# Kernel optimization log

Measured on AMD Instinct MI355X. Metric: run time of the kernel, lower is better.

The kernel has to match this reference:

```python
import jax, jax.numpy as jnp
import numpy as np

NUM_EMBEDDINGS = 1024
EMBEDDING_DIM = 64
DECAY = 0.99
EPS = 1e-5


def setup_inputs() -> dict:
    key = jax.random.key(0)
    k0, k1, k2 = jax.random.split(key, 3)
    return {
        "inputs": jax.random.normal(k0, (32, 64, 64, EMBEDDING_DIM), dtype=jnp.float32),
        "embeddings": jax.random.normal(k1, (NUM_EMBEDDINGS, EMBEDDING_DIM), dtype=jnp.float32),
        "ema_cluster_size": jnp.ones((NUM_EMBEDDINGS,), dtype=jnp.float32),
        "ema_w": jax.random.normal(k2, (NUM_EMBEDDINGS, EMBEDDING_DIM), dtype=jnp.float32),
    }


def reference(inputs, embeddings, ema_cluster_size, ema_w):
    input_shape = inputs.shape
    flat = inputs.reshape(-1, EMBEDDING_DIM)  # [N, D]

    input_sq = jnp.sum(flat * flat, axis=1, keepdims=True)          # [N, 1]
    codebook_sq = jnp.sum(embeddings * embeddings, axis=1)          # [K]
    dot = jnp.matmul(flat, embeddings.T)                            # [N, K]
    distances = input_sq + codebook_sq - 2.0 * dot

    encoding_indices = jnp.argmin(distances, axis=-1)               # [N]
    encodings = jax.nn.one_hot(encoding_indices, NUM_EMBEDDINGS, dtype=flat.dtype)  # [N, K]
    quantized_flat = jnp.take(embeddings, encoding_indices, axis=0)  # [N, D]

    # --- EMA updates (training path) ---
    current_counts = jax.ops.segment_sum(
        jnp.ones_like(encoding_indices, dtype=flat.dtype),
        encoding_indices, num_segments=NUM_EMBEDDINGS)              # == sum(encodings, 0)
    upd_cluster = ema_cluster_size * DECAY + (1.0 - DECAY) * current_counts
    n = jnp.sum(upd_cluster)
    upd_cluster = (upd_cluster + EPS) / (n + NUM_EMBEDDINGS * EPS) * n

    # sum of inputs assigned to each code == encodings.T @ flat
    assignment_sums = jax.ops.segment_sum(flat, encoding_indices,
                                          num_segments=NUM_EMBEDDINGS)  # [K, D]
    upd_ema_w = ema_w * DECAY + (1.0 - DECAY) * assignment_sums
    upd_embeddings = upd_ema_w / (upd_cluster[:, None] + EPS)

    quantization_loss = jnp.mean((flat - quantized_flat) ** 2).reshape((1,))
    quantized = quantized_flat.reshape(input_shape)
    quantized_flow = inputs + jax.lax.stop_gradient(quantized - inputs)

    usage_counts = current_counts
    usage_ratio = jnp.sum((usage_counts > 0).astype(jnp.float32)) / NUM_EMBEDDINGS

    return (quantized_flow, encodings, usage_ratio, quantization_loss,
            upd_embeddings, upd_cluster, upd_ema_w)
```

## Files before the change

### kernel.cpp

```cpp
#include <hip/hip_runtime.h>
#include <hip/hip_bf16.h>

#define NK 1024
#define ND 64
#define NV 131072
#define BR 128
#define DECAY_F 0.99f
#define OMD_F 0.01f
#define EPS_F 1e-5f
#define KEPS_F 0.01024f

typedef const __attribute__((address_space(1))) void* gas1_t;
typedef __attribute__((address_space(3))) void* las3_t;
#define GLOAD_LDS16(gp, lp) \
    __builtin_amdgcn_global_load_lds((gas1_t)(gp), (las3_t)(lp), 16, 0, 0)


__global__ __launch_bounds__(256) void vq_prep(const float* __restrict__ emb,
                                               float* __restrict__ csq,
                                               int* __restrict__ cnt,
                                               double* loss,
                                               float4* __restrict__ acc4)
{
    int k = blockIdx.x * 256 + threadIdx.x;
    cnt[k] = 0;
    if (k == 0) *loss = 0.0;
    float4 z = make_float4(0.f, 0.f, 0.f, 0.f);
#pragma unroll
    for (int i = 0; i < 16; ++i) acc4[k + i * 1024] = z;
    float p[ND];
    const float4* e4 = reinterpret_cast<const float4*>(emb + (size_t)k * ND);
#pragma unroll
    for (int i = 0; i < 16; ++i) {
        float4 v = e4[i];
        p[4*i+0] = __fmul_rn(v.x, v.x);
        p[4*i+1] = __fmul_rn(v.y, v.y);
        p[4*i+2] = __fmul_rn(v.z, v.z);
        p[4*i+3] = __fmul_rn(v.w, v.w);
    }
    float r[8];
#pragma unroll
    for (int j = 0; j < 8; ++j) r[j] = p[j];
#pragma unroll
    for (int i = 8; i < ND; i += 8)
#pragma unroll
        for (int j = 0; j < 8; ++j) r[j] = __fadd_rn(r[j], p[i+j]);
    csq[k] = __fadd_rn(__fadd_rn(__fadd_rn(r[0], r[1]), __fadd_rn(r[2], r[3])),
                       __fadd_rn(__fadd_rn(r[4], r[5]), __fadd_rn(r[6], r[7])));
}

__global__ __launch_bounds__(256, 2) void vq_assign(
    const float* __restrict__ x_in, const float* __restrict__ emb,
    const float* __restrict__ csq, float* __restrict__ out_qf,
    float* __restrict__ out_enc, int* __restrict__ indices,
    int* __restrict__ cnt, double* __restrict__ loss_acc)
{
    __shared__ __align__(16) float xs[BR * ND];
    __shared__ __align__(16) float es[128 * ND];
    __shared__ float csq_s[NK];
    __shared__ float isq_s[BR];
    __shared__ double lds_ls[4];

    const int tid  = threadIdx.x;
    const int lane = tid & 63;
    const int wv   = tid >> 6;
    const int tx   = tid & 15;
    const int ty   = tid >> 4;
    const int txs  = tx & 7;
    const int tys  = ty & 7;
    const size_t rowbase = (size_t)blockIdx.x * BR;

#pragma unroll
    for (int c = 0; c < 8; ++c) {
        int f = tid + c * 256;
        int row = f >> 4, ch = f & 15;
        int sch = ch ^ (row & 7);
        GLOAD_LDS16(x_in + rowbase * ND + row * ND + sch * 4, &xs[f * 4]);
    }
#pragma unroll
    for (int c = 0; c < 8; ++c) {
        int f = tid + c * 256;
        int row = f >> 4, ch = f & 15;
        int sch = ch ^ (row & 7);
        GLOAD_LDS16(emb + (size_t)row * ND + sch * 4, &es[f * 4]);
    }
#pragma unroll
    for (int c = 0; c < 4; ++c) csq_s[tid + c * 256] = csq[tid + c * 256];
    __syncthreads();

    if (tid < BR) {
        const int rs = tid & 7;
        const float* xr = &xs[tid * ND];
        float r[8];
        {
            float4 a = *(const float4*)&xr[(0 ^ rs) * 4];
            float4 b = *(const float4*)&xr[(1 ^ rs) * 4];
            r[0] = __fmul_rn(a.x, a.x); r[1] = __fmul_rn(a.y, a.y);
            r[2] = __fmul_rn(a.z, a.z); r[3] = __fmul_rn(a.w, a.w);
            r[4] = __fmul_rn(b.x, b.x); r[5] = __fmul_rn(b.y, b.y);
            r[6] = __fmul_rn(b.z, b.z); r[7] = __fmul_rn(b.w, b.w);
        }
#pragma unroll
        for (int g = 1; g < 8; ++g) {
            float4 a = *(const float4*)&xr[((2*g)   ^ rs) * 4];
            float4 b = *(const float4*)&xr[((2*g+1) ^ rs) * 4];
            r[0] = __fadd_rn(r[0], __fmul_rn(a.x, a.x));
            r[1] = __fadd_rn(r[1], __fmul_rn(a.y, a.y));
            r[2] = __fadd_rn(r[2], __fmul_rn(a.z, a.z));
            r[3] = __fadd_rn(r[3], __fmul_rn(a.w, a.w));
            r[4] = __fadd_rn(r[4], __fmul_rn(b.x, b.x));
            r[5] = __fadd_rn(r[5], __fmul_rn(b.y, b.y));
            r[6] = __fadd_rn(r[6], __fmul_rn(b.z, b.z));
            r[7] = __fadd_rn(r[7], __fmul_rn(b.w, b.w));
        }
        isq_s[tid] = __fadd_rn(__fadd_rn(__fadd_rn(r[0], r[1]), __fadd_rn(r[2], r[3])),
                               __fadd_rn(__fadd_rn(r[4], r[5]), __fadd_rn(r[6], r[7])));
    }

    float best[8];
    int   bestk[8];
#pragma unroll
    for (int i = 0; i < 8; ++i) { best[i] = 3.4e38f; bestk[i] = 0; }

    for (int t = 0; t < 8; ++t) {
        float acc[8][8];
#pragma unroll
        for (int i = 0; i < 8; ++i)
#pragma unroll
            for (int j = 0; j < 8; ++j) acc[i][j] = 0.f;

        for (int ch = 0; ch < 16; ++ch) {
            const int xo = (ch ^ tys) * 4;
            const int eo = (ch ^ txs) * 4;
            float4 xf[8], ef[8];
#pragma unroll
            for (int i = 0; i < 8; ++i)
                xf[i] = *(const float4*)&xs[(ty + 16*i) * ND + xo];
#pragma unroll
            for (int j = 0; j < 8; ++j)
                ef[j] = *(const float4*)&es[(tx + 16*j) * ND + eo];
#pragma unroll
            for (int i = 0; i < 8; ++i) {
#pragma unroll
                for (int j = 0; j < 8; ++j) {
                    float a = acc[i][j];
                    a = __builtin_fmaf(xf[i].x, ef[j].x, a);
                    a = __builtin_fmaf(xf[i].y, ef[j].y, a);
                    a = __builtin_fmaf(xf[i].z, ef[j].z, a);
                    a = __builtin_fmaf(xf[i].w, ef[j].w, a);
                    acc[i][j] = a;
                }
            }
        }

#pragma unroll
        for (int i = 0; i < 8; ++i) {
            float isq = isq_s[ty + 16*i];
#pragma unroll
            for (int j = 0; j < 8; ++j) {
                float dist = __fsub_rn(__fadd_rn(isq, csq_s[t * 128 + tx + 16*j]),
                                       __fmul_rn(2.0f, acc[i][j]));
                if (dist < best[i]) { best[i] = dist; bestk[i] = t * 128 + tx + 16*j; }
            }
        }

        {
            int rl = t * 16 + wv * 4;
#pragma unroll
            for (int rr = 0; rr < 4; ++rr) {
                float4* dst = reinterpret_cast<float4*>(out_enc + (rowbase + rl + rr) * NK);
                float4 z = make_float4(0.f, 0.f, 0.f, 0.f);
#pragma unroll
                for (int jj = 0; jj < 4; ++jj) dst[jj * 64 + lane] = z;
            }
        }

        __syncthreads();
        if (t < 7) {
#pragma unroll
            for (int c = 0; c < 8; ++c) {
                int f = tid + c * 256;
                int row = f >> 4, ch = f & 15;
                int sch = ch ^ (row & 7);
                GLOAD_LDS16(emb + (size_t)(t + 1) * 128 * ND + row * ND + sch * 4,
                            &es[f * 4]);
            }
        }
        __syncthreads();
    }

    float* red_d = es;
    int*   red_i = reinterpret_cast<int*>(es + 2048);
#pragma unroll
    for (int i = 0; i < 8; ++i) {
        red_d[(ty + 16*i) * 16 + tx] = best[i];
        red_i[(ty + 16*i) * 16 + tx] = bestk[i];
    }
    __syncthreads();
    if (tid < BR) {
        float bd = red_d[tid * 16];
        int   bk = red_i[tid * 16];
#pragma unroll
        for (int c = 1; c < 16; ++c) {
            float d  = red_d[tid * 16 + c];
            int   k2 = red_i[tid * 16 + c];
            if (d < bd || (d == bd && k2 < bk)) { bd = d; bk = k2; }
        }
        size_t grow = rowbase + tid;
        indices[grow] = bk;
        out_enc[grow * NK + bk] = 1.0f;
        atomicAdd(&cnt[bk], 1);
        red_i[tid * 16] = bk;
    }
    __syncthreads();

    float lsum = 0.f;
    const int lsw = ((lane >> 2)) ;
    for (int r = 0; r < 32; ++r) {
        int rl = wv * 32 + r;
        int kr = red_i[rl * 16];
        size_t grow = rowbase + rl;
        float xv = xs[rl * ND + ((lsw ^ (rl & 7)) << 2) + (lane & 3)];
        float ev = emb[(size_t)kr * ND + lane];
        out_qf[grow * ND + lane] = __fadd_rn(xv, __fsub_rn(ev, xv));
        float dd = __fsub_rn(xv, ev);
        lsum = __builtin_fmaf(dd, dd, lsum);
    }
    double ls = (double)lsum;
#pragma unroll
    for (int off = 32; off >= 1; off >>= 1) ls += __shfl_xor(ls, off, 64);
    if (lane == 0) lds_ls[wv] = ls;
    __syncthreads();
    if (tid == 0)
        atomicAdd(loss_acc, (lds_ls[0] + lds_ls[1]) + (lds_ls[2] + lds_ls[3]));
}

__global__ __launch_bounds__(256) void vq_scan(
    const int* __restrict__ cnt, const float* __restrict__ ema_cs,
    const double* __restrict__ loss_acc, float* __restrict__ ucf_ws,
    int* __restrict__ base, int* __restrict__ cursor,
    float* __restrict__ out_uc, float* __restrict__ out_usage,
    float* __restrict__ out_loss)
{
    __shared__ float uc_s[1024];
    __shared__ int   wsum[4];
    __shared__ int   usage_s;
    __shared__ float n_s;
    const int tid  = threadIdx.x;
    const int lane = tid & 63;
    const int wv   = tid >> 6;
    if (tid == 0) usage_s = 0;
    __syncthreads();

    int c4[4];
    int ucount = 0;
#pragma unroll
    for (int j = 0; j < 4; ++j) {
        int k = tid * 4 + j;
        int c = cnt[k];
        c4[j] = c;
        if (c > 0) ucount++;
        uc_s[k] = __fadd_rn(__fmul_rn(ema_cs[k], DECAY_F), __fmul_rn(OMD_F, (float)c));
    }
    atomicAdd(&usage_s, ucount);
    __syncthreads();

    if (tid < 64) {
        int b = tid >> 3, j = tid & 7;
        float r = uc_s[b * 128 + j];
#pragma unroll
        for (int i = 1; i < 16; ++i)
            r = __fadd_rn(r, uc_s[b * 128 + 8 * i + j]);
        r = __fadd_rn(r, __shfl_xor(r, 1, 64));
        r = __fadd_rn(r, __shfl_xor(r, 2, 64));
        r = __fadd_rn(r, __shfl_xor(r, 4, 64));
        r = __fadd_rn(r, __shfl_xor(r, 8, 64));
        r = __fadd_rn(r, __shfl_xor(r, 16, 64));
        r = __fadd_rn(r, __shfl_xor(r, 32, 64));
        if (tid == 0) {
            n_s = r;
            *out_usage = __fdiv_rn((float)usage_s, 1024.0f);
            *out_loss  = (float)(*loss_acc / 8388608.0);
        }
    }
    __syncthreads();

    const float n = n_s;
#pragma unroll
    for (int j = 0; j < 4; ++j) {
        int k = tid * 4 + j;
        float ucfv = __fmul_rn(__fdiv_rn(__fadd_rn(uc_s[k], EPS_F), __fadd_rn(n, KEPS_F)), n);
        out_uc[k] = ucfv;
        ucf_ws[k] = ucfv;
    }

    int s = c4[0] + c4[1] + c4[2] + c4[3];
    int incl = s;
#pragma unroll
    for (int off = 1; off < 64; off <<= 1) {
        int v = __shfl_up(incl, off, 64);
        if (lane >= off) incl += v;
    }
    if (lane == 63) wsum[wv] = incl;
    __syncthreads();
    int woff = 0;
    for (int w = 0; w < wv; ++w) woff += wsum[w];
    int run = woff + incl - s;
#pragma unroll
    for (int j = 0; j < 4; ++j) {
        int k = tid * 4 + j;
        base[k] = run; cursor[k] = run;
        run += c4[j];
    }
}

__global__ __launch_bounds__(256) void vq_scatter(
    const int* __restrict__ idx, int* __restrict__ cursor,
    int* __restrict__ rows, int* __restrict__ codes)
{
    int i = blockIdx.x * 256 + threadIdx.x;
    int k = idx[i];
    int slot = atomicAdd(&cursor[k], 1);
    rows[slot] = i;
    codes[slot] = k;
}

__global__ __launch_bounds__(256) void vq_gather(
    const float* __restrict__ x_in, const int* __restrict__ rows,
    const int* __restrict__ codes, float* __restrict__ acc_buf)
{
    const int lane = threadIdx.x & 63;
    const int wv   = threadIdx.x >> 6;
    const int seg  = blockIdx.x * 4 + wv;
    const int g    = seg * 64;

    const int rid = rows[g + lane];
    const int kc  = codes[g + lane];

    float acc = 0.f;
    for (int e8 = 0; e8 < 8; ++e8) {
        float xv[8];
#pragma unroll
        for (int u = 0; u < 8; ++u) {
            int r = __shfl(rid, e8 * 8 + u, 64);
            xv[u] = x_in[(size_t)r * ND + lane];
        }
#pragma unroll
        for (int u = 0; u < 8; ++u) {
            int e = e8 * 8 + u;
            int k = __shfl(kc, e, 64);
            acc = __fadd_rn(acc, xv[u]);
            int knext = __shfl(kc, (e + 1) & 63, 64);
            if (e == 63) knext = -1;
            if (k != knext) {
                atomicAdd(&acc_buf[(size_t)k * ND + lane], acc);
                acc = 0.f;
            }
        }
    }
}

__global__ __launch_bounds__(256) void vq_final(
    const float* __restrict__ acc_buf, const float* __restrict__ ema_w,
    const float* __restrict__ ucf, float* __restrict__ out_updw,
    float* __restrict__ out_upde)
{
    int gid = blockIdx.x * 256 + threadIdx.x;
    int k = gid >> 6;
    float w = __fadd_rn(__fmul_rn(ema_w[gid], DECAY_F), __fmul_rn(OMD_F, acc_buf[gid]));
    out_updw[gid] = w;
    out_upde[gid] = __fdiv_rn(w, __fadd_rn(ucf[k], EPS_F));
}

extern "C" void kernel_launch(void* const* d_in, const int* in_sizes, int n_in,
                              void* d_out, int out_size, void* d_ws, size_t ws_size,
                              hipStream_t stream)
{
    const float* x_in   = (const float*)d_in[0];
    const float* emb    = (const float*)d_in[1];
    const float* ema_cs = (const float*)d_in[2];
    const float* ema_w  = (const float*)d_in[3];

    float* out_qf    = (float*)d_out;
    float* out_enc   = out_qf + (size_t)NV * ND;
    float* out_usage = out_enc + (size_t)NV * NK;
    float* out_loss  = out_usage + 1;
    float* out_upde  = out_loss + 1;
    float* out_uc    = out_upde + (size_t)NK * ND;
    float* out_updw  = out_uc + NK;

    char* ws = (char*)d_ws;
    float*  ws_csq    = (float*)(ws);
    int*    ws_cnt    = (int*)(ws + 4096);
    int*    ws_base   = (int*)(ws + 8192);
    int*    ws_cursor = (int*)(ws + 12288);
    float*  ws_ucf    = (float*)(ws + 16384);
    double* ws_loss   = (double*)(ws + 20480);
    int*    ws_idx    = (int*)(ws + 24576);
    int*    ws_rows   = (int*)(ws + 24576 + (size_t)NV * 4);
    int*    ws_codes  = (int*)(ws + 24576 + (size_t)NV * 8);
    float*  ws_acc    = (float*)(ws + 24576 + (size_t)NV * 12);

    vq_prep<<<4, 256, 0, stream>>>(emb, ws_csq, ws_cnt, ws_loss, (float4*)ws_acc);
    vq_assign<<<NV / BR, 256, 0, stream>>>(x_in, emb, ws_csq, out_qf, out_enc,
                                           ws_idx, ws_cnt, ws_loss);
    vq_scan<<<1, 256, 0, stream>>>(ws_cnt, ema_cs, ws_loss, ws_ucf, ws_base,
                                   ws_cursor, out_uc, out_usage, out_loss);
    vq_scatter<<<NV / 256, 256, 0, stream>>>(ws_idx, ws_cursor, ws_rows, ws_codes);
    vq_gather<<<512, 256, 0, stream>>>(x_in, ws_rows, ws_codes, ws_acc);
    vq_final<<<256, 256, 0, stream>>>(ws_acc, ema_w, ws_ucf, out_updw, out_upde);
}
```

Before: 322.2 us.

## Fuse per-code input sums into assign kernel via atomics, drop scatter/gather

Removes the scan-offset, scatter and gather kernels and accumulates assigned inputs into the per-code sum buffer with float atomics directly in the assign epilogue. It also moves the one-hot zero fill from inside the codebook tile loop into the epilogue, writing each row's zeros before setting the 1.0 after a memory wait and barrier. This cuts two launches and the re-read of inputs. In exchange it adds contended global float atomics and changes the order of floating-point summation.

Measured after the change: 300.0 us. 1.07x faster.

```diff
diff --git a/kernel.cpp b/kernel.cpp
--- a/kernel.cpp
+++ b/kernel.cpp
@@ -52,7 +52,7 @@
 __global__ __launch_bounds__(256, 2) void vq_assign(
     const float* __restrict__ x_in, const float* __restrict__ emb,
     const float* __restrict__ csq, float* __restrict__ out_qf,
-    float* __restrict__ out_enc, int* __restrict__ indices,
+    float* __restrict__ out_enc, float* __restrict__ acc_buf,
     int* __restrict__ cnt, double* __restrict__ loss_acc)
 {
     __shared__ __align__(16) float xs[BR * ND];
@@ -164,17 +164,6 @@
             }
         }
 
-        {
-            int rl = t * 16 + wv * 4;
-#pragma unroll
-            for (int rr = 0; rr < 4; ++rr) {
-                float4* dst = reinterpret_cast<float4*>(out_enc + (rowbase + rl + rr) * NK);
-                float4 z = make_float4(0.f, 0.f, 0.f, 0.f);
-#pragma unroll
-                for (int jj = 0; jj < 4; ++jj) dst[jj * 64 + lane] = z;
-            }
-        }
-
         __syncthreads();
         if (t < 7) {
 #pragma unroll
@@ -206,31 +195,40 @@
             int   k2 = red_i[tid * 16 + c];
             if (d < bd || (d == bd && k2 < bk)) { bd = d; bk = k2; }
         }
-        size_t grow = rowbase + tid;
-        indices[grow] = bk;
-        out_enc[grow * NK + bk] = 1.0f;
         atomicAdd(&cnt[bk], 1);
         red_i[tid * 16] = bk;
     }
     __syncthreads();
 
     float lsum = 0.f;
-    const int lsw = ((lane >> 2)) ;
+    const int lsw = (lane >> 2);
+    const float4 zv = make_float4(0.f, 0.f, 0.f, 0.f);
     for (int r = 0; r < 32; ++r) {
         int rl = wv * 32 + r;
         int kr = red_i[rl * 16];
         size_t grow = rowbase + rl;
+        float4* dst = reinterpret_cast<float4*>(out_enc + grow * NK);
+#pragma unroll
+        for (int jj = 0; jj < 4; ++jj) dst[jj * 64 + lane] = zv;
         float xv = xs[rl * ND + ((lsw ^ (rl & 7)) << 2) + (lane & 3)];
         float ev = emb[(size_t)kr * ND + lane];
         out_qf[grow * ND + lane] = __fadd_rn(xv, __fsub_rn(ev, xv));
         float dd = __fsub_rn(xv, ev);
         lsum = __builtin_fmaf(dd, dd, lsum);
+        atomicAdd(&acc_buf[(size_t)kr * ND + lane], xv);
     }
     double ls = (double)lsum;
 #pragma unroll
     for (int off = 32; off >= 1; off >>= 1) ls += __shfl_xor(ls, off, 64);
     if (lane == 0) lds_ls[wv] = ls;
-    __syncthreads();
+
+    asm volatile("s_waitcnt vmcnt(0)" ::: "memory");
+    __syncthreads();
+
+    if (tid < BR) {
+        int bk = red_i[tid * 16];
+        out_enc[(rowbase + tid) * NK + bk] = 1.0f;
+    }
     if (tid == 0)
         atomicAdd(loss_acc, (lds_ls[0] + lds_ls[1]) + (lds_ls[2] + lds_ls[3]));
 }
@@ -238,27 +236,21 @@
 __global__ __launch_bounds__(256) void vq_scan(
     const int* __restrict__ cnt, const float* __restrict__ ema_cs,
     const double* __restrict__ loss_acc, float* __restrict__ ucf_ws,
-    int* __restrict__ base, int* __restrict__ cursor,
     float* __restrict__ out_uc, float* __restrict__ out_usage,
     float* __restrict__ out_loss)
 {
     __shared__ float uc_s[1024];
-    __shared__ int   wsum[4];
     __shared__ int   usage_s;
     __shared__ float n_s;
     const int tid  = threadIdx.x;
-    const int lane = tid & 63;
-    const int wv   = tid >> 6;
     if (tid == 0) usage_s = 0;
     __syncthreads();
 
-    int c4[4];
     int ucount = 0;
 #pragma unroll
     for (int j = 0; j < 4; ++j) {
         int k = tid * 4 + j;
         int c = cnt[k];
-        c4[j] = c;
         if (c > 0) ucount++;
         uc_s[k] = __fadd_rn(__fmul_rn(ema_cs[k], DECAY_F), __fmul_rn(OMD_F, (float)c));
     }
@@ -293,71 +285,6 @@
         out_uc[k] = ucfv;
         ucf_ws[k] = ucfv;
     }
-
-    int s = c4[0] + c4[1] + c4[2] + c4[3];
-    int incl = s;
-#pragma unroll
-    for (int off = 1; off < 64; off <<= 1) {
-        int v = __shfl_up(incl, off, 64);
-        if (lane >= off) incl += v;
-    }
-    if (lane == 63) wsum[wv] = incl;
-    __syncthreads();
-    int woff = 0;
-    for (int w = 0; w < wv; ++w) woff += wsum[w];
-    int run = woff + incl - s;
-#pragma unroll
-    for (int j = 0; j < 4; ++j) {
-        int k = tid * 4 + j;
-        base[k] = run; cursor[k] = run;
-        run += c4[j];
-    }
-}
-
-__global__ __launch_bounds__(256) void vq_scatter(
-    const int* __restrict__ idx, int* __restrict__ cursor,
-    int* __restrict__ rows, int* __restrict__ codes)
-{
-    int i = blockIdx.x * 256 + threadIdx.x;
-    int k = idx[i];
-    int slot = atomicAdd(&cursor[k], 1);
-    rows[slot] = i;
-    codes[slot] = k;
-}
-
-__global__ __launch_bounds__(256) void vq_gather(
-    const float* __restrict__ x_in, const int* __restrict__ rows,
-    const int* __restrict__ codes, float* __restrict__ acc_buf)
-{
-    const int lane = threadIdx.x & 63;
-    const int wv   = threadIdx.x >> 6;
-    const int seg  = blockIdx.x * 4 + wv;
-    const int g    = seg * 64;
-
-    const int rid = rows[g + lane];
-    const int kc  = codes[g + lane];
-
-    float acc = 0.f;
-    for (int e8 = 0; e8 < 8; ++e8) {
-        float xv[8];
-#pragma unroll
-        for (int u = 0; u < 8; ++u) {
-            int r = __shfl(rid, e8 * 8 + u, 64);
-            xv[u] = x_in[(size_t)r * ND + lane];
-        }
-#pragma unroll
-        for (int u = 0; u < 8; ++u) {
-            int e = e8 * 8 + u;
-            int k = __shfl(kc, e, 64);
-            acc = __fadd_rn(acc, xv[u]);
-            int knext = __shfl(kc, (e + 1) & 63, 64);
-            if (e == 63) knext = -1;
-            if (k != knext) {
-                atomicAdd(&acc_buf[(size_t)k * ND + lane], acc);
-                acc = 0.f;
-            }
-        }
-    }
 }
 
 __global__ __launch_bounds__(256) void vq_final(
@@ -392,21 +319,14 @@
     char* ws = (char*)d_ws;
     float*  ws_csq    = (float*)(ws);
     int*    ws_cnt    = (int*)(ws + 4096);
-    int*    ws_base   = (int*)(ws + 8192);
-    int*    ws_cursor = (int*)(ws + 12288);
     float*  ws_ucf    = (float*)(ws + 16384);
     double* ws_loss   = (double*)(ws + 20480);
-    int*    ws_idx    = (int*)(ws + 24576);
-    int*    ws_rows   = (int*)(ws + 24576 + (size_t)NV * 4);
-    int*    ws_codes  = (int*)(ws + 24576 + (size_t)NV * 8);
-    float*  ws_acc    = (float*)(ws + 24576 + (size_t)NV * 12);
+    float*  ws_acc    = (float*)(ws + 1597440);
 
     vq_prep<<<4, 256, 0, stream>>>(emb, ws_csq, ws_cnt, ws_loss, (float4*)ws_acc);
     vq_assign<<<NV / BR, 256, 0, stream>>>(x_in, emb, ws_csq, out_qf, out_enc,
-                                           ws_idx, ws_cnt, ws_loss);
-    vq_scan<<<1, 256, 0, stream>>>(ws_cnt, ema_cs, ws_loss, ws_ucf, ws_base,
-                                   ws_cursor, out_uc, out_usage, out_loss);
-    vq_scatter<<<NV / 256, 256, 0, stream>>>(ws_idx, ws_cursor, ws_rows, ws_codes);
-    vq_gather<<<512, 256, 0, stream>>>(x_in, ws_rows, ws_codes, ws_acc);
+                                           ws_acc, ws_cnt, ws_loss);
+    vq_scan<<<1, 256, 0, stream>>>(ws_cnt, ema_cs, ws_loss, ws_ucf,
+                                   out_uc, out_usage, out_loss);
     vq_final<<<256, 256, 0, stream>>>(ws_acc, ema_w, ws_ucf, out_updw, out_upde);
 }
```
